# Kernel optimization log

Hardware: AMD Instinct MI355X
Metric: run time of the kernel (lower is better)

Reference implementation:

```python
import jax, jax.numpy as jnp
import numpy as np

N_HEADS = 8
TANH_CLIP = 10.0
NEG = -1e9  # finite stand-in for -inf so log_softmax/vjp stay NaN-free


def setup_inputs() -> dict:
    key = jax.random.key(0)
    ks = jax.random.split(key, 8)
    B, N, D = 256, 1000, 128
    embeddings = jax.random.normal(ks[0], (B, N, D), dtype=jnp.float32)
    W_node = jax.random.normal(ks[1], (D, 3 * D), dtype=jnp.float32) * (1.0 / np.sqrt(D))
    W_fixed = jax.random.normal(ks[2], (D, D), dtype=jnp.float32) * (1.0 / np.sqrt(D))
    W_step = jax.random.normal(ks[3], (2 * D, D), dtype=jnp.float32) * (1.0 / np.sqrt(2 * D))
    W_out = jax.random.normal(ks[4], (D, D), dtype=jnp.float32) * (1.0 / np.sqrt(D))
    first_idx = jax.random.randint(ks[5], (B,), 0, N)
    last_idx = jax.random.randint(ks[6], (B,), 0, N)
    mask = jax.random.randint(ks[7], (B, N), 0, 2).astype(jnp.bool_)
    mask = mask.at[:, 0].set(False)  # guarantee at least one feasible node
    return {"embeddings": embeddings, "W_node": W_node, "W_fixed": W_fixed,
            "W_step": W_step, "W_out": W_out, "first_idx": first_idx,
            "last_idx": last_idx, "mask": mask}


def reference(embeddings, W_node, W_fixed, W_step, W_out, first_idx, last_idx, mask):
    # One pointer-network decode step (TSP variant of AttentionModel._get_log_p),
    # including the _precompute projections.
    B, N, D = embeddings.shape
    H = N_HEADS
    dk = D // H

    # _precompute: fixed context + glimpse K/V + logit key
    graph_embed = embeddings.mean(axis=1)                       # [B, D]
    fixed_ctx = graph_embed @ W_fixed                           # [B, D]
    kvl = embeddings @ W_node                                   # [B, N, 3D]
    K, V, logit_K = jnp.split(kvl, 3, axis=-1)                  # each [B, N, D]

    # step context: cat(first-node emb, last-node emb) -> project to D
    b = jnp.arange(B)
    step_ctx = jnp.concatenate([embeddings[b, first_idx], embeddings[b, last_idx]], axis=-1)  # [B, 2D]
    q = fixed_ctx + step_ctx @ W_step                           # [B, D]

    # masked multi-head glimpse attention (q_len = 1)
    qh = q.reshape(B, H, dk)                                    # [B, H, dk]
    Kh = K.reshape(B, N, H, dk)
    Vh = V.reshape(B, N, H, dk)
    compat = jnp.einsum('bhd,bnhd->bhn', qh, Kh) / np.sqrt(dk)  # [B, H, N]
    compat = jnp.where(mask[:, None, :], NEG, compat)           # mask_inner
    attn = jax.nn.softmax(compat, axis=-1)
    heads = jnp.einsum('bhn,bnhd->bhd', attn, Vh)               # [B, H, dk]
    glimpse = heads.reshape(B, D) @ W_out                       # [B, D]

    # single-head logit attention with tanh clipping
    logits = jnp.einsum('bd,bnd->bn', glimpse, logit_K) / np.sqrt(D)  # [B, N]
    logits = jnp.tanh(logits) * TANH_CLIP
    logits = jnp.where(mask, NEG, logits)                       # mask_logits
    return jax.nn.log_softmax(logits, axis=-1)                  # [B, N]
```

## Files before the change

kernel.cpp:

```cpp
#include <hip/hip_runtime.h>


#define NEG (-1e9f)

__device__ __forceinline__ float rfl(float x) {
    return __int_as_float(__builtin_amdgcn_readfirstlane(__float_as_int(x)));
}

__global__ __launch_bounds__(1024) void k_fused(
    const float* __restrict__ E, const float* __restrict__ Wn,
    const float* __restrict__ Wf, const float* __restrict__ Ws,
    const float* __restrict__ Wo,
    const int* __restrict__ fi, const int* __restrict__ li,
    const int* __restrict__ maskI, const unsigned char* __restrict__ maskB,
    float* __restrict__ out)
{
    const int b = blockIdx.x;
    const int t = threadIdx.x;

    __shared__ float4 Et[4096];
    __shared__ float4 qk4[256];
    __shared__ float4 pt4[256];
    __shared__ float4 EbarF4[256];
    __shared__ float4 mu4[32], e14[32], e24[32], gp4[32];
    __shared__ float q[128], heads[128], gl[128];
    __shared__ float qred[8][128];
    __shared__ float mh[8], lh[8];
    __shared__ float red[16];
    __shared__ float stat[2];
    __shared__ int flagS;

    float* const mu = (float*)mu4;
    float* const e1 = (float*)e14;
    float* const e2 = (float*)e24;
    float* const gp = (float*)gp4;
    float* const pt = (float*)pt4;
    float* const EbarF = (float*)EbarF4;
    float* const qkf = (float*)qk4;
    float* const qrf = (float*)qred;

    const float4* E4 = (const float4*)(E + (size_t)b * 128000);

    if (t == 0) flagS = 0;
    const uint4 dv = ((const uint4*)maskI)[t];
    const unsigned det = (dv.x | dv.y | dv.z | dv.w) & 0xFFFFFF00u;

    const int rr = t >> 3, qq = t & 7;
    const int c4 = t & 31, sl = t >> 5;
    const int wv = t >> 6;

    {
        const int cm = t & 31, sm = t >> 5;
        float4 acc = make_float4(0.f, 0.f, 0.f, 0.f);
        for (int r = sm; r < 1000; r += 32) {
            const float4 v = E4[r * 32 + cm];
            acc.x += v.x; acc.y += v.y; acc.z += v.z; acc.w += v.w;
        }
        Et[t] = acc;
    }
    if (t >= 512 && t < 544) {
        e14[t - 512] = E4[fi[b] * 32 + (t - 512)];
    } else if (t >= 544 && t < 576) {
        e24[t - 544] = E4[li[b] * 32 + (t - 544)];
    }
    __syncthreads();
    if (det) atomicOr(&flagS, 1);
    if (t < 32) {
        float4 acc = Et[t];
        #pragma unroll
        for (int s = 1; s < 32; ++s) {
            const float4 v = Et[s * 32 + t];
            acc.x += v.x; acc.y += v.y; acc.z += v.z; acc.w += v.w;
        }
        const float inv = 1.0f / 1000.0f;
        mu4[t] = make_float4(acc.x * inv, acc.y * inv, acc.z * inv, acc.w * inv);
    }
    __syncthreads();

    {
        const int part = t >> 7, d = t & 127;
        float acc = 0.f;
        const int k0 = part * 48;
        for (int k = k0; k < k0 + 48; ++k) {
            const float s = (k < 128) ? mu[k] : (k < 256 ? e1[k - 128] : e2[k - 256]);
            const float w = (k < 128) ? Wf[k * 128 + d] : Ws[(k - 128) * 128 + d];
            acc += s * w;
        }
        qred[part][d] = acc;
    }
    __syncthreads();
    if (t < 128) {
        float acc = 0.f;
        #pragma unroll
        for (int p = 0; p < 8; ++p) acc += qred[p][t];
        q[t] = acc;
    }
    __syncthreads();
    {
        const int j = t & 127, cg = t >> 7;
        const float qj = q[j];
        for (int c0 = 0; c0 < 128; c0 += 8) {
            const int c = c0 + cg;
            float v = Wn[c * 384 + j] * qj;
            v += __shfl_down(v, 8, 16);
            v += __shfl_down(v, 4, 16);
            v += __shfl_down(v, 2, 16);
            v += __shfl_down(v, 1, 16);
            if ((j & 15) == 0) {
                const int h = j >> 4, s = c >> 2;
                qkf[h * 128 + (s ^ (s >> 2)) * 4 + (c & 3)] = v * 0.25f;
            }
        }
    }
    __syncthreads();

    const bool useB = (flagS != 0);

    float s_m[8], s_l[8];
    #pragma unroll
    for (int h = 0; h < 8; ++h) { s_m[h] = -3e38f; s_l[h] = 0.f; }
    float4 eacc[8];
    #pragma unroll
    for (int h = 0; h < 8; ++h) eacc[h] = make_float4(0.f, 0.f, 0.f, 0.f);

    for (int tile = 0; tile < 8; ++tile) {
        const int g = tile * 128 + rr;
        float pch[8];
        #pragma unroll
        for (int h = 0; h < 8; ++h) pch[h] = 0.f;
        {
            float4 v[4];
            if (g < 1000) {
                #pragma unroll
                for (int i = 0; i < 4; ++i) v[i] = E4[g * 32 + qq * 4 + i];
            } else {
                #pragma unroll
                for (int i = 0; i < 4; ++i) v[i] = make_float4(0.f, 0.f, 0.f, 0.f);
            }
            #pragma unroll
            for (int i = 0; i < 4; ++i) {
                const int grp = qq * 4 + i;
                Et[rr * 32 + (grp ^ (rr & 7))] = v[i];
                const int sg = grp ^ (grp >> 2);
                #pragma unroll
                for (int h = 0; h < 8; ++h) {
                    const float4 w = qk4[h * 32 + sg];
                    pch[h] += v[i].x * w.x + v[i].y * w.y + v[i].z * w.z + v[i].w * w.w;
                }
            }
        }
        #pragma unroll
        for (int m = 1; m <= 4; m <<= 1) {
            #pragma unroll
            for (int h = 0; h < 8; ++h) pch[h] += __shfl_xor(pch[h], m, 64);
        }
        bool msk = (g >= 1000);
        if (!msk) msk = useB ? (maskB[b * 1000 + g] != 0)
                             : (maskI[b * 1000 + g] != 0);
        if (msk) {
            #pragma unroll
            for (int h = 0; h < 8; ++h) pch[h] = NEG;
        }
        float al[8];
        #pragma unroll
        for (int h = 0; h < 8; ++h) {
            float x = pch[h];
            x = fmaxf(x, __shfl_xor(x, 8, 64));
            x = fmaxf(x, __shfl_xor(x, 16, 64));
            x = fmaxf(x, __shfl_xor(x, 32, 64));
            const float mn = rfl(fmaxf(s_m[h], x));
            al[h] = __expf(s_m[h] - mn);
            s_m[h] = mn;
        }
        float e[8];
        #pragma unroll
        for (int h = 0; h < 8; ++h) {
            e[h] = __expf(pch[h] - s_m[h]);
            float x = e[h];
            x += __shfl_xor(x, 8, 64);
            x += __shfl_xor(x, 16, 64);
            x += __shfl_xor(x, 32, 64);
            s_l[h] = rfl(s_l[h] * al[h] + x);
        }
        if (qq == 0)      pt4[rr * 2]     = make_float4(e[0], e[1], e[2], e[3]);
        else if (qq == 1) pt4[rr * 2 + 1] = make_float4(e[4], e[5], e[6], e[7]);
        asm volatile("s_waitcnt lgkmcnt(0)" ::: "memory");
        #pragma unroll
        for (int h = 0; h < 8; ++h) {
            eacc[h].x *= al[h]; eacc[h].y *= al[h];
            eacc[h].z *= al[h]; eacc[h].w *= al[h];
        }
        #pragma unroll
        for (int j = 0; j < 4; ++j) {
            const int r = sl * 4 + j;
            const float4 ev = Et[r * 32 + (c4 ^ (r & 7))];
            const float4 p0 = pt4[r * 2];
            const float4 p1 = pt4[r * 2 + 1];
            eacc[0].x += p0.x * ev.x; eacc[0].y += p0.x * ev.y; eacc[0].z += p0.x * ev.z; eacc[0].w += p0.x * ev.w;
            eacc[1].x += p0.y * ev.x; eacc[1].y += p0.y * ev.y; eacc[1].z += p0.y * ev.z; eacc[1].w += p0.y * ev.w;
            eacc[2].x += p0.z * ev.x; eacc[2].y += p0.z * ev.y; eacc[2].z += p0.z * ev.z; eacc[2].w += p0.z * ev.w;
            eacc[3].x += p0.w * ev.x; eacc[3].y += p0.w * ev.y; eacc[3].z += p0.w * ev.z; eacc[3].w += p0.w * ev.w;
            eacc[4].x += p1.x * ev.x; eacc[4].y += p1.x * ev.y; eacc[4].z += p1.x * ev.z; eacc[4].w += p1.x * ev.w;
            eacc[5].x += p1.y * ev.x; eacc[5].y += p1.y * ev.y; eacc[5].z += p1.y * ev.z; eacc[5].w += p1.y * ev.w;
            eacc[6].x += p1.z * ev.x; eacc[6].y += p1.z * ev.y; eacc[6].z += p1.z * ev.z; eacc[6].w += p1.z * ev.w;
            eacc[7].x += p1.w * ev.x; eacc[7].y += p1.w * ev.y; eacc[7].z += p1.w * ev.z; eacc[7].w += p1.w * ev.w;
        }
        asm volatile("" ::: "memory");
    }

    if ((t & 63) == 0) {
        #pragma unroll
        for (int h = 0; h < 8; ++h) {
            qrf[wv * 32 + h] = s_m[h];
            qrf[wv * 32 + 8 + h] = s_l[h];
        }
    }
    __syncthreads();
    if (t < 8) {
        float m = qrf[t];
        for (int w2 = 1; w2 < 16; ++w2) m = fmaxf(m, qrf[w2 * 32 + t]);
        mh[t] = m;
    }
    __syncthreads();
    if (t < 128) {
        const int w2 = t >> 3, h = t & 7;
        const float f = __expf(qrf[w2 * 32 + h] - mh[h]);
        qrf[w2 * 32 + 16 + h] = f;
        qrf[w2 * 32 + 24 + h] = qrf[w2 * 32 + 8 + h] * f;
    }
    __syncthreads();
    if (t < 8) {
        float s = 0.f;
        for (int w2 = 0; w2 < 16; ++w2) s += qrf[w2 * 32 + 24 + t];
        lh[t] = s;
    }
    {
        float fw[8];
        #pragma unroll
        for (int h = 0; h < 8; ++h) fw[h] = qrf[wv * 32 + 16 + h];
        #pragma unroll
        for (int h = 0; h < 8; ++h) {
            eacc[h].x *= fw[h]; eacc[h].y *= fw[h];
            eacc[h].z *= fw[h]; eacc[h].w *= fw[h];
        }
    }
    __syncthreads();

    if (sl >= 16) {
        #pragma unroll
        for (int h = 0; h < 8; ++h) Et[(sl - 16) * 256 + h * 32 + c4] = eacc[h];
    }
    __syncthreads();
    if (sl < 16) {
        #pragma unroll
        for (int h = 0; h < 8; ++h) {
            const float4 o = Et[sl * 256 + h * 32 + c4];
            eacc[h].x += o.x; eacc[h].y += o.y; eacc[h].z += o.z; eacc[h].w += o.w;
            Et[sl * 256 + h * 32 + c4] = eacc[h];
        }
    }
    __syncthreads();
    if (t < 256) {
        const int h = t >> 5, cc = t & 31;
        float4 s = make_float4(0.f, 0.f, 0.f, 0.f);
        #pragma unroll
        for (int s2 = 0; s2 < 16; ++s2) {
            const float4 v = Et[s2 * 256 + h * 32 + cc];
            s.x += v.x; s.y += v.y; s.z += v.z; s.w += v.w;
        }
        const float invl = 1.0f / lh[h];
        EbarF4[h * 32 + cc] = make_float4(s.x * invl, s.y * invl, s.z * invl, s.w * invl);
    }
    __syncthreads();

    {
        const int part = t >> 7, d = t & 127, h = d >> 4;
        float acc = 0.f;
        const int c0 = part * 16;
        for (int c = c0; c < c0 + 16; ++c) acc += EbarF[h * 128 + c] * Wn[c * 384 + 128 + d];
        qred[part][d] = acc;
    }
    __syncthreads();
    if (t < 128) {
        float acc = 0.f;
        #pragma unroll
        for (int p = 0; p < 8; ++p) acc += qred[p][t];
        heads[t] = acc;
    }
    __syncthreads();
    {
        const int part = t >> 7, d = t & 127;
        float acc = 0.f;
        const int j0 = part * 16;
        for (int j = j0; j < j0 + 16; ++j) acc += heads[j] * Wo[j * 128 + d];
        qred[part][d] = acc;
    }
    __syncthreads();
    if (t < 128) {
        float acc = 0.f;
        #pragma unroll
        for (int p = 0; p < 8; ++p) acc += qred[p][t];
        gl[t] = acc;
    }
    __syncthreads();
    {
        const int part = t >> 7, c = t & 127;
        float acc = 0.f;
        const int d0 = part * 16;
        for (int d = d0; d < d0 + 16; ++d) acc += Wn[c * 384 + 256 + d] * gl[d];
        qred[part][c] = acc;
    }
    __syncthreads();
    if (t < 128) {
        float acc = 0.f;
        #pragma unroll
        for (int p = 0; p < 8; ++p) acc += qred[p][t];
        gp[t] = acc * 0.08838834764831845f;
    }
    __syncthreads();

    for (int tile = 0; tile < 8; ++tile) {
        const int g = tile * 128 + rr;
        float acc = 0.f;
        if (g < 1000) {
            #pragma unroll
            for (int i = 0; i < 4; ++i) {
                const float4 v = E4[g * 32 + qq * 4 + i];
                const float4 w = gp4[qq * 4 + i];
                acc += v.x * w.x + v.y * w.y + v.z * w.z + v.w * w.w;
            }
        }
        acc += __shfl_xor(acc, 1, 64);
        acc += __shfl_xor(acc, 2, 64);
        acc += __shfl_xor(acc, 4, 64);
        if (qq == 0 && g < 1000) {
            float zz = 10.0f * tanhf(acc);
            const bool m = useB ? (maskB[b * 1000 + g] != 0)
                                : (maskI[b * 1000 + g] != 0);
            if (m) zz = NEG;
            pt[g] = zz;
        }
    }
    __syncthreads();
    float v = (t < 1000) ? pt[t] : -3e38f;
    #pragma unroll
    for (int off = 32; off > 0; off >>= 1) v = fmaxf(v, __shfl_down(v, off, 64));
    if ((t & 63) == 0) red[t >> 6] = v;
    __syncthreads();
    if (t == 0) {
        float m = red[0];
        for (int i = 1; i < 16; ++i) m = fmaxf(m, red[i]);
        stat[0] = m;
    }
    __syncthreads();
    float sv = (t < 1000) ? __expf(pt[t] - stat[0]) : 0.f;
    #pragma unroll
    for (int off = 32; off > 0; off >>= 1) sv += __shfl_down(sv, off, 64);
    if ((t & 63) == 0) red[t >> 6] = sv;
    __syncthreads();
    if (t == 0) {
        float s = 0.f;
        for (int i = 0; i < 16; ++i) s += red[i];
        stat[1] = stat[0] + __logf(s);
    }
    __syncthreads();
    if (t < 1000)
        out[(size_t)b * 1000 + t] = pt[t] - stat[1];
}

extern "C" void kernel_launch(void* const* d_in, const int* in_sizes, int n_in,
                              void* d_out, int out_size, void* d_ws, size_t ws_size,
                              hipStream_t stream) {
    const float* E  = (const float*)d_in[0];
    const float* Wn = (const float*)d_in[1];
    const float* Wf = (const float*)d_in[2];
    const float* Ws = (const float*)d_in[3];
    const float* Wo = (const float*)d_in[4];
    const int*   fi = (const int*)d_in[5];
    const int*   li = (const int*)d_in[6];
    const int*   maskI = (const int*)d_in[7];
    const unsigned char* maskB = (const unsigned char*)d_in[7];
    float* out = (float*)d_out;

    k_fused<<<256, 1024, 0, stream>>>(E, Wn, Wf, Ws, Wo, fi, li, maskI, maskB, out);
}
```

Measured before the change: 288.4 us.

## Double-buffer embedding tiles via async global-to-LDS loads in attention loop

Replaces per-tile register loads plus LDS stores of embedding rows with global_load_lds direct-to-LDS copies into a double buffer, prefetching the next tile while the current one is computed. Mask loads are hoisted out of the tile loop into a per-thread additive bias array. The XOR swizzle on the LDS tile is dropped because the async copy writes linearly, which may bring back bank conflicts, and LDS use doubles. Out-of-range rows are clamped to row 999 and rely on the additive mask to be ignored.

```diff
diff --git a/kernel.cpp b/kernel.cpp
--- a/kernel.cpp
+++ b/kernel.cpp
@@ -5,6 +5,12 @@
 
 __device__ __forceinline__ float rfl(float x) {
     return __int_as_float(__builtin_amdgcn_readfirstlane(__float_as_int(x)));
+}
+
+__device__ __forceinline__ void gld16(const float4* g, float4* l) {
+    __builtin_amdgcn_global_load_lds(
+        (const __attribute__((address_space(1))) void*)g,
+        (__attribute__((address_space(3))) void*)l, 16, 0, 0);
 }
 
 __global__ __launch_bounds__(1024) void k_fused(
@@ -18,7 +24,7 @@
     const int b = blockIdx.x;
     const int t = threadIdx.x;
 
-    __shared__ float4 Et[4096];
+    __shared__ float4 Et[8192];
     __shared__ float4 qk4[256];
     __shared__ float4 pt4[256];
     __shared__ float4 EbarF4[256];
@@ -48,6 +54,7 @@
     const int rr = t >> 3, qq = t & 7;
     const int c4 = t & 31, sl = t >> 5;
     const int wv = t >> 6;
+    const int lane = t & 63;
 
     {
         const int cm = t & 31, sm = t >> 5;
@@ -116,6 +123,15 @@
 
     const bool useB = (flagS != 0);
 
+    float madd[8];
+    #pragma unroll
+    for (int tl = 0; tl < 8; ++tl) {
+        const int g = tl * 128 + rr;
+        bool m = (g >= 1000);
+        if (!m) m = useB ? (maskB[b * 1000 + g] != 0) : (maskI[b * 1000 + g] != 0);
+        madd[tl] = m ? -2e9f : 0.f;
+    }
+
     float s_m[8], s_l[8];
     #pragma unroll
     for (int h = 0; h < 8; ++h) { s_m[h] = -3e38f; s_l[h] = 0.f; }
@@ -123,30 +139,46 @@
     #pragma unroll
     for (int h = 0; h < 8; ++h) eacc[h] = make_float4(0.f, 0.f, 0.f, 0.f);
 
+    {
+        const int g0 = wv * 8;
+        #pragma unroll
+        for (int j = 0; j < 4; ++j) {
+            int eidx = g0 * 32 + j * 64 + lane;
+            const int row = eidx >> 5;
+            if (row > 999) eidx -= (row - 999) << 5;
+            gld16(E4 + eidx, Et + (size_t)wv * 256 + j * 64);
+        }
+    }
+
     for (int tile = 0; tile < 8; ++tile) {
-        const int g = tile * 128 + rr;
+        float4* const B = Et + (tile & 1) * 4096;
+        if (tile < 7) {
+            asm volatile("s_waitcnt lgkmcnt(0)" ::: "memory");
+            float4* const Bn = Et + ((tile + 1) & 1) * 4096;
+            const int g0 = (tile + 1) * 128 + wv * 8;
+            #pragma unroll
+            for (int j = 0; j < 4; ++j) {
+                int eidx = g0 * 32 + j * 64 + lane;
+                const int row = eidx >> 5;
+                if (row > 999) eidx -= (row - 999) << 5;
+                gld16(E4 + eidx, Bn + (size_t)wv * 256 + j * 64);
+            }
+            asm volatile("s_waitcnt vmcnt(4)" ::: "memory");
+        } else {
+            asm volatile("s_waitcnt vmcnt(0)" ::: "memory");
+        }
         float pch[8];
         #pragma unroll
         for (int h = 0; h < 8; ++h) pch[h] = 0.f;
-        {
-            float4 v[4];
-            if (g < 1000) {
-                #pragma unroll
-                for (int i = 0; i < 4; ++i) v[i] = E4[g * 32 + qq * 4 + i];
-            } else {
-                #pragma unroll
-                for (int i = 0; i < 4; ++i) v[i] = make_float4(0.f, 0.f, 0.f, 0.f);
-            }
+        #pragma unroll
+        for (int i = 0; i < 4; ++i) {
+            const int grp = qq * 4 + i;
+            const float4 ev = B[rr * 32 + grp];
+            const int sg = grp ^ (grp >> 2);
             #pragma unroll
-            for (int i = 0; i < 4; ++i) {
-                const int grp = qq * 4 + i;
-                Et[rr * 32 + (grp ^ (rr & 7))] = v[i];
-                const int sg = grp ^ (grp >> 2);
-                #pragma unroll
-                for (int h = 0; h < 8; ++h) {
-                    const float4 w = qk4[h * 32 + sg];
-                    pch[h] += v[i].x * w.x + v[i].y * w.y + v[i].z * w.z + v[i].w * w.w;
-                }
+            for (int h = 0; h < 8; ++h) {
+                const float4 w = qk4[h * 32 + sg];
+                pch[h] += ev.x * w.x + ev.y * w.y + ev.z * w.z + ev.w * w.w;
             }
         }
         #pragma unroll
@@ -154,13 +186,8 @@
             #pragma unroll
             for (int h = 0; h < 8; ++h) pch[h] += __shfl_xor(pch[h], m, 64);
         }
-        bool msk = (g >= 1000);
-        if (!msk) msk = useB ? (maskB[b * 1000 + g] != 0)
-                             : (maskI[b * 1000 + g] != 0);
-        if (msk) {
-            #pragma unroll
-            for (int h = 0; h < 8; ++h) pch[h] = NEG;
-        }
+        #pragma unroll
+        for (int h = 0; h < 8; ++h) pch[h] += madd[tile];
         float al[8];
         #pragma unroll
         for (int h = 0; h < 8; ++h) {
@@ -193,7 +220,7 @@
         #pragma unroll
         for (int j = 0; j < 4; ++j) {
             const int r = sl * 4 + j;
-            const float4 ev = Et[r * 32 + (c4 ^ (r & 7))];
+            const float4 ev = B[r * 32 + c4];
             const float4 p0 = pt4[r * 2];
             const float4 p1 = pt4[r * 2 + 1];
             eacc[0].x += p0.x * ev.x; eacc[0].y += p0.x * ev.y; eacc[0].z += p0.x * ev.z; eacc[0].w += p0.x * ev.w;
```

Measured after the change: 297.6 us. +3.2%, slower.
